# Kernel tuning notes

Hardware: AMD Instinct MI355X
Metric: run time of the kernel (lower is better)

## Reference

```python
import jax, jax.numpy as jnp
import numpy as np

I_FEAT = 4096
O_FEAT = 4096
BATCH = 8192


def setup_inputs() -> dict:
    key = jax.random.key(0)
    k1, k2, k3 = jax.random.split(key, 3)
    x_input = jax.random.normal(k1, (BATCH, I_FEAT), dtype=jnp.float32)
    toeplitz_params = jax.random.normal(k2, (O_FEAT + I_FEAT - 1,), dtype=jnp.float32) * (1.0 / np.sqrt(I_FEAT))
    bias = jax.random.normal(k3, (O_FEAT,), dtype=jnp.float32) * (1.0 / np.sqrt(I_FEAT))
    return {"x_input": x_input, "toeplitz_params": toeplitz_params, "bias": bias}


def _toeplitz(params, out_features, in_features):
    # row i, col j -> params[(out_features - 1 - i) + j]
    i = jnp.arange(out_features)[:, None]
    j = jnp.arange(in_features)[None, :]
    return params[(out_features - 1) - i + j]  # [O, I]


def reference(x_input, toeplitz_params, bias):
    weight = _toeplitz(toeplitz_params, O_FEAT, I_FEAT)  # [O, I]
    # x.mm(weight.t()) + bias
    return jnp.einsum('bi,oi->bo', x_input, weight) + bias[None, :]
```

## Files before the change

### kernel.cpp

```cpp
#include <hip/hip_runtime.h>

typedef __attribute__((ext_vector_type(4))) int i32x4;
typedef __attribute__((ext_vector_type(4))) float f32x4;

#define AS1 __attribute__((address_space(1)))
#define AS3 __attribute__((address_space(3)))

constexpr int MDIM = 8192;
constexpr int NDIM = 4096;
constexpr int KDIM = 4096;

constexpr int BM = 256, BN = 256, BKB = 128;
constexpr int NKT = KDIM / BKB;

__device__ __forceinline__ void gld_lds16(const signed char* g, signed char* l) {
  __builtin_amdgcn_global_load_lds((const AS1 void*)g, (AS3 void*)l, 16, 0, 0);
}

__device__ __forceinline__ int q8(float v, float inv) {
  int q = __float2int_rn(v * inv);
  return q;
}

__global__ void wscale_kernel(const float* __restrict__ params, float* __restrict__ swbuf) {
  int t = (int)threadIdx.x;
  float m = 0.f;
  for (int i = t; i < NDIM + KDIM - 1; i += 256) m = fmaxf(m, fabsf(params[i]));
#pragma unroll
  for (int off = 32; off >= 1; off >>= 1) m = fmaxf(m, __shfl_xor(m, off));
  __shared__ float red[4];
  if ((t & 63) == 0) red[t >> 6] = m;
  __syncthreads();
  if (t == 0) {
    m = fmaxf(fmaxf(red[0], red[1]), fmaxf(red[2], red[3]));
    m = fmaxf(m, 1e-30f);
    swbuf[0] = m * (1.0f / 127.0f);
    swbuf[1] = 127.0f / m;
  }
}

__global__ __launch_bounds__(256) void quant_x_kernel(
    const float* __restrict__ x, signed char* __restrict__ xq, float* __restrict__ sxr) {
  int row = (int)blockIdx.x;
  int t = (int)threadIdx.x;
  const float4* px = (const float4*)(x + (size_t)row * KDIM) + t * 4;
  float4 v[4];
#pragma unroll
  for (int i = 0; i < 4; ++i) v[i] = px[i];
  float m = 0.f;
#pragma unroll
  for (int i = 0; i < 4; ++i)
    m = fmaxf(fmaxf(fmaxf(fabsf(v[i].x), fabsf(v[i].y)), fmaxf(fabsf(v[i].z), fabsf(v[i].w))), m);
#pragma unroll
  for (int off = 32; off >= 1; off >>= 1) m = fmaxf(m, __shfl_xor(m, off));
  __shared__ float red[4];
  if ((t & 63) == 0) red[t >> 6] = m;
  __syncthreads();
  m = fmaxf(fmaxf(red[0], red[1]), fmaxf(red[2], red[3]));
  m = fmaxf(m, 1e-30f);
  float inv = 127.0f / m;
  if (t == 0) sxr[row] = m * (1.0f / 127.0f);
  i32x4 w;
#pragma unroll
  for (int i = 0; i < 4; ++i) {
    int q0 = q8(v[i].x, inv), q1 = q8(v[i].y, inv), q2 = q8(v[i].z, inv), q3 = q8(v[i].w, inv);
    w[i] = (q0 & 0xff) | ((q1 & 0xff) << 8) | ((q2 & 0xff) << 16) | ((q3 & 0xff) << 24);
  }
  *(i32x4*)(xq + (size_t)row * KDIM + t * 16) = w;
}

__global__ __launch_bounds__(256) void build_wq_kernel(
    const float* __restrict__ params, const float* __restrict__ swbuf,
    signed char* __restrict__ wq) {
  float inv = swbuf[1];
  int i = blockIdx.x * 256 + (int)threadIdx.x;
  int o = i >> 8;
  int k0 = (i & 255) << 4;
  const float* p = params + (NDIM - 1 - o + k0);
  i32x4 w;
#pragma unroll
  for (int j = 0; j < 4; ++j) {
    int q0 = q8(p[4 * j + 0], inv), q1 = q8(p[4 * j + 1], inv);
    int q2 = q8(p[4 * j + 2], inv), q3 = q8(p[4 * j + 3], inv);
    w[j] = (q0 & 0xff) | ((q1 & 0xff) << 8) | ((q2 & 0xff) << 16) | ((q3 & 0xff) << 24);
  }
  *(i32x4*)(wq + (size_t)o * KDIM + k0) = w;
}

__global__ __launch_bounds__(512, 2) void toep_gemm_i8(
    const signed char* __restrict__ A,
    const signed char* __restrict__ Bw,
    const float* __restrict__ bias,
    const float* __restrict__ sxr,
    const float* __restrict__ swbuf,
    float* __restrict__ C)
{
  __shared__ signed char sA[2][BM * BKB];
  __shared__ signed char sB[2][BN * BKB];

  constexpr int NBM = MDIM / BM;
  constexpr int NBN = NDIM / BN;
  constexpr int NWG = NBM * NBN;
  int bid = (int)blockIdx.x;
  int swz = (bid & 7) * (NWG >> 3) + (bid >> 3);
  int bm = swz / NBN, bn = swz % NBN;
  int m0 = bm * BM, n0 = bn * BN;

  int t = (int)threadIdx.x;
  int lane = t & 63, wid = t >> 6;
  int wm = wid >> 2, wn = wid & 3;
  int lr = lane & 15, lk = lane >> 4;

  int scol = (((t & 7) ^ ((t >> 3) & 7)) << 4);
  const signed char* gA = A + (size_t)(m0 + (t >> 3)) * KDIM + scol;
  const signed char* gB = Bw + (size_t)(n0 + (t >> 3)) * KDIM + scol;

#define STG_A(c, kt, R0) gld_lds16(gA + (size_t)(R0) * KDIM + (kt) * BKB, &sA[c][(R0) * BKB + t * 16])
#define STG_B(c, kt, R0) gld_lds16(gB + (size_t)(R0) * KDIM + (kt) * BKB, &sB[c][(R0) * BKB + t * 16])

  int aswz = (lr & 7) << 4;
  int c0 = (lk * 16) ^ aswz;
  int c1 = (64 + lk * 16) ^ aswz;

  i32x4 av[4][2], bvA[2][2], bvB[2][2];
  i32x4 acc[8][4];
#pragma unroll
  for (int i = 0; i < 8; ++i)
#pragma unroll
    for (int j = 0; j < 4; ++j) acc[i][j] = (i32x4){0, 0, 0, 0};

#define LDA_SUB(c, msub) do { \
  _Pragma("unroll") \
  for (int mi = 0; mi < 4; ++mi) { \
    const signed char* p_ = &sA[c][(wm * 128 + (msub) * 64 + mi * 16 + lr) * BKB]; \
    av[mi][0] = *(const i32x4*)(p_ + c0); \
    av[mi][1] = *(const i32x4*)(p_ + c1); \
  } } while (0)

#define LDB_GRP(c, nsub, BV) do { \
  _Pragma("unroll") \
  for (int ni = 0; ni < 2; ++ni) { \
    const signed char* p_ = &sB[c][(wn * 64 + (nsub) * 32 + ni * 16 + lr) * BKB]; \
    BV[ni][0] = *(const i32x4*)(p_ + c0); \
    BV[ni][1] = *(const i32x4*)(p_ + c1); \
  } } while (0)

#define MMA_Q(msub, nsub, BV) do { \
  __builtin_amdgcn_s_setprio(1); \
  _Pragma("unroll") \
  for (int mi = 0; mi < 4; ++mi) \
    _Pragma("unroll") \
    for (int ni = 0; ni < 2; ++ni) { \
      acc[(msub) * 4 + mi][(nsub) * 2 + ni] = __builtin_amdgcn_mfma_i32_16x16x64_i8( \
          av[mi][0], BV[ni][0], acc[(msub) * 4 + mi][(nsub) * 2 + ni], 0, 0, 0); \
      acc[(msub) * 4 + mi][(nsub) * 2 + ni] = __builtin_amdgcn_mfma_i32_16x16x64_i8( \
          av[mi][1], BV[ni][1], acc[(msub) * 4 + mi][(nsub) * 2 + ni], 0, 0, 0); \
    } \
  __builtin_amdgcn_s_setprio(0); \
} while (0)

#define SB0() __builtin_amdgcn_sched_barrier(0)
#define BAR() __builtin_amdgcn_s_barrier()

  STG_B(0, 0, 0); STG_B(0, 0, 64); STG_B(0, 0, 128); STG_B(0, 0, 192);
  STG_A(0, 0, 0); STG_A(0, 0, 64); STG_A(0, 0, 128); STG_A(0, 0, 192);
  asm volatile("s_waitcnt vmcnt(0)" ::: "memory");
  BAR();

#define TILE(c, kt) do { \
  const bool st_ = (kt) + 1 < NKT; \
  if (st_) { \
    STG_B((c) ^ 1, (kt) + 1, 0); STG_B((c) ^ 1, (kt) + 1, 64); \
    STG_B((c) ^ 1, (kt) + 1, 128); STG_B((c) ^ 1, (kt) + 1, 192); \
    STG_A((c) ^ 1, (kt) + 1, 0); STG_A((c) ^ 1, (kt) + 1, 64); \
    STG_A((c) ^ 1, (kt) + 1, 128); STG_A((c) ^ 1, (kt) + 1, 192); \
  } \
  LDA_SUB(c, 0); LDB_GRP(c, 0, bvA); SB0(); \
  LDB_GRP(c, 1, bvB); \
  asm volatile("s_waitcnt lgkmcnt(4)" ::: "memory"); SB0(); \
  MMA_Q(0, 0, bvA); \
  asm volatile("s_waitcnt lgkmcnt(0)" ::: "memory"); SB0(); \
  MMA_Q(0, 1, bvB); \
  LDA_SUB(c, 1); \
  asm volatile("s_waitcnt lgkmcnt(0)" ::: "memory"); SB0(); \
  MMA_Q(1, 1, bvB); \
  MMA_Q(1, 0, bvA); \
  asm volatile("s_waitcnt vmcnt(0)" ::: "memory"); \
  BAR(); \
} while (0)

  for (int kt = 0; kt < NKT; kt += 2) {
    TILE(0, kt);
    TILE(1, kt + 1);
  }

  float sw = swbuf[0];
  float bvv[4];
#pragma unroll
  for (int fn = 0; fn < 4; ++fn) bvv[fn] = bias[n0 + wn * 64 + fn * 16 + lr];
#pragma unroll
  for (int fm = 0; fm < 8; ++fm) {
    int row0 = m0 + wm * 128 + fm * 16 + lk * 4;
    float sx_[4];
#pragma unroll
    for (int r = 0; r < 4; ++r) sx_[r] = sxr[row0 + r] * sw;
#pragma unroll
    for (int fn = 0; fn < 4; ++fn) {
      int col = n0 + wn * 64 + fn * 16 + lr;
#pragma unroll
      for (int r = 0; r < 4; ++r)
        C[(size_t)(row0 + r) * NDIM + col] = (float)acc[fm][fn][r] * sx_[r] + bvv[fn];
    }
  }
#undef TILE
#undef MMA_Q
#undef LDB_GRP
#undef LDA_SUB
#undef STG_A
#undef STG_B
#undef SB0
#undef BAR
}

__global__ __launch_bounds__(256) void toep_f32_fallback(
    const float* __restrict__ X, const float* __restrict__ P,
    const float* __restrict__ bias, float* __restrict__ C)
{
  constexpr int TM = 64, TN = 64, TK = 32;
  __shared__ float xs[TM][TK + 1];
  __shared__ float win[TN + TK];
  int bm = blockIdx.x / (NDIM / TN);
  int bn = blockIdx.x % (NDIM / TN);
  int m0 = bm * TM, n0 = bn * TN;
  int t = (int)threadIdx.x;
  int tx = t & 15, ty = t >> 4;
  float acc[4][4] = {};
  for (int k0 = 0; k0 < KDIM; k0 += TK) {
    __syncthreads();
    for (int i = t; i < TM * TK; i += 256) {
      int r = i >> 5, c = i & 31;
      xs[r][c] = X[(size_t)(m0 + r) * KDIM + k0 + c];
    }
    if (t < TN + TK - 1) win[t] = P[(NDIM - 1) - n0 - (TN - 1) + k0 + t];
    __syncthreads();
    for (int kk = 0; kk < TK; ++kk) {
      float xv[4];
#pragma unroll
      for (int i = 0; i < 4; ++i) xv[i] = xs[ty * 4 + i][kk];
#pragma unroll
      for (int j = 0; j < 4; ++j) {
        float wv = win[kk + (TN - 1) - (tx * 4 + j)];
#pragma unroll
        for (int i = 0; i < 4; ++i) acc[i][j] += xv[i] * wv;
      }
    }
  }
#pragma unroll
  for (int i = 0; i < 4; ++i)
#pragma unroll
    for (int j = 0; j < 4; ++j)
      C[(size_t)(m0 + ty * 4 + i) * NDIM + n0 + tx * 4 + j] = acc[i][j] + bias[n0 + tx * 4 + j];
}

extern "C" void kernel_launch(void* const* d_in, const int* in_sizes, int n_in,
                              void* d_out, int out_size, void* d_ws, size_t ws_size,
                              hipStream_t stream) {
  const float* x = (const float*)d_in[0];
  const float* params = (const float*)d_in[1];
  const float* bias = (const float*)d_in[2];
  float* out = (float*)d_out;

  const size_t xq_off = 0;
  const size_t wq_off = (size_t)MDIM * KDIM;
  const size_t sx_off = wq_off + (size_t)NDIM * KDIM;
  const size_t sw_off = sx_off + (size_t)MDIM * 4;
  const size_t need = sw_off + 64;

  if (ws_size >= need) {
    signed char* xq = (signed char*)d_ws + xq_off;
    signed char* wq = (signed char*)d_ws + wq_off;
    float* sxr = (float*)((char*)d_ws + sx_off);
    float* swbuf = (float*)((char*)d_ws + sw_off);
    wscale_kernel<<<1, 256, 0, stream>>>(params, swbuf);
    quant_x_kernel<<<MDIM, 256, 0, stream>>>(x, xq, sxr);
    build_wq_kernel<<<NDIM * KDIM / 16 / 256, 256, 0, stream>>>(params, swbuf, wq);
    toep_gemm_i8<<<(MDIM / BM) * (NDIM / BN), 512, 0, stream>>>(xq, wq, bias, sxr, swbuf, out);
  } else {
    toep_f32_fallback<<<(MDIM / 64) * (NDIM / 64), 256, 0, stream>>>(x, params, bias, out);
  }
}
```

Baseline: 175.9 us.

## Prefetch next tile's LDS fragments across barrier and interleave global staging with MFMA

Adds a second A-fragment register set so the first A/B fragments of the next k-tile are read from LDS right after the barrier, overlapping with the last MFMA quadrant of the current tile. The global-to-LDS staging loads are split into B and A halves placed between MFMA quadrants rather than issued all at once at the start of the tile. The goal is to hide LDS read latency and spread memory issue across compute. In exchange it raises VGPR pressure, which could reduce occupancy or cause spills. The vmcnt waits also become tighter to get right.

Result: no change. 173.6 us (-1.3%).

```diff
diff --git a/kernel.cpp b/kernel.cpp
--- a/kernel.cpp
+++ b/kernel.cpp
@@ -18,8 +18,7 @@
 }
 
 __device__ __forceinline__ int q8(float v, float inv) {
-  int q = __float2int_rn(v * inv);
-  return q;
+  return __float2int_rn(v * inv);
 }
 
 __global__ void wscale_kernel(const float* __restrict__ params, float* __restrict__ swbuf) {
@@ -122,19 +121,20 @@
   int c0 = (lk * 16) ^ aswz;
   int c1 = (64 + lk * 16) ^ aswz;
 
-  i32x4 av[4][2], bvA[2][2], bvB[2][2];
+  i32x4 avA[4][2], avB[4][2];
+  i32x4 bvA[2][2], bvB[2][2];
   i32x4 acc[8][4];
 #pragma unroll
   for (int i = 0; i < 8; ++i)
 #pragma unroll
     for (int j = 0; j < 4; ++j) acc[i][j] = (i32x4){0, 0, 0, 0};
 
-#define LDA_SUB(c, msub) do { \
+#define LDA_GRP(c, msub, AV) do { \
   _Pragma("unroll") \
   for (int mi = 0; mi < 4; ++mi) { \
     const signed char* p_ = &sA[c][(wm * 128 + (msub) * 64 + mi * 16 + lr) * BKB]; \
-    av[mi][0] = *(const i32x4*)(p_ + c0); \
-    av[mi][1] = *(const i32x4*)(p_ + c1); \
+    AV[mi][0] = *(const i32x4*)(p_ + c0); \
+    AV[mi][1] = *(const i32x4*)(p_ + c1); \
   } } while (0)
 
 #define LDB_GRP(c, nsub, BV) do { \
@@ -145,16 +145,16 @@
     BV[ni][1] = *(const i32x4*)(p_ + c1); \
   } } while (0)
 
-#define MMA_Q(msub, nsub, BV) do { \
+#define MMA_Q(msub, nsub, AV, BV) do { \
   __builtin_amdgcn_s_setprio(1); \
   _Pragma("unroll") \
   for (int mi = 0; mi < 4; ++mi) \
     _Pragma("unroll") \
     for (int ni = 0; ni < 2; ++ni) { \
       acc[(msub) * 4 + mi][(nsub) * 2 + ni] = __builtin_amdgcn_mfma_i32_16x16x64_i8( \
-          av[mi][0], BV[ni][0], acc[(msub) * 4 + mi][(nsub) * 2 + ni], 0, 0, 0); \
+          AV[mi][0], BV[ni][0], acc[(msub) * 4 + mi][(nsub) * 2 + ni], 0, 0, 0); \
       acc[(msub) * 4 + mi][(nsub) * 2 + ni] = __builtin_amdgcn_mfma_i32_16x16x64_i8( \
-          av[mi][1], BV[ni][1], acc[(msub) * 4 + mi][(nsub) * 2 + ni], 0, 0, 0); \
+          AV[mi][1], BV[ni][1], acc[(msub) * 4 + mi][(nsub) * 2 + ni], 0, 0, 0); \
     } \
   __builtin_amdgcn_s_setprio(0); \
 } while (0)
@@ -166,27 +166,33 @@
   STG_A(0, 0, 0); STG_A(0, 0, 64); STG_A(0, 0, 128); STG_A(0, 0, 192);
   asm volatile("s_waitcnt vmcnt(0)" ::: "memory");
   BAR();
+  LDA_GRP(0, 0, avA); LDB_GRP(0, 0, bvA);
+  SB0();
 
 #define TILE(c, kt) do { \
   const bool st_ = (kt) + 1 < NKT; \
-  if (st_) { \
-    STG_B((c) ^ 1, (kt) + 1, 0); STG_B((c) ^ 1, (kt) + 1, 64); \
-    STG_B((c) ^ 1, (kt) + 1, 128); STG_B((c) ^ 1, (kt) + 1, 192); \
-    STG_A((c) ^ 1, (kt) + 1, 0); STG_A((c) ^ 1, (kt) + 1, 64); \
-    STG_A((c) ^ 1, (kt) + 1, 128); STG_A((c) ^ 1, (kt) + 1, 192); \
-  } \
-  LDA_SUB(c, 0); LDB_GRP(c, 0, bvA); SB0(); \
+   \
   LDB_GRP(c, 1, bvB); \
+  if (st_) { STG_B((c) ^ 1, (kt) + 1, 0); STG_B((c) ^ 1, (kt) + 1, 64); \
+             STG_B((c) ^ 1, (kt) + 1, 128); STG_B((c) ^ 1, (kt) + 1, 192); } \
+  SB0(); \
   asm volatile("s_waitcnt lgkmcnt(4)" ::: "memory"); SB0(); \
-  MMA_Q(0, 0, bvA); \
+  MMA_Q(0, 0, avA, bvA); \
+   \
+  LDA_GRP(c, 1, avB); \
+  if (st_) { STG_A((c) ^ 1, (kt) + 1, 0); STG_A((c) ^ 1, (kt) + 1, 64); \
+             STG_A((c) ^ 1, (kt) + 1, 128); STG_A((c) ^ 1, (kt) + 1, 192); } \
+  SB0(); \
+  asm volatile("s_waitcnt lgkmcnt(8)" ::: "memory"); SB0(); \
+  MMA_Q(0, 1, avA, bvB); \
+   \
   asm volatile("s_waitcnt lgkmcnt(0)" ::: "memory"); SB0(); \
-  MMA_Q(0, 1, bvB); \
-  LDA_SUB(c, 1); \
-  asm volatile("s_waitcnt lgkmcnt(0)" ::: "memory"); SB0(); \
-  MMA_Q(1, 1, bvB); \
-  MMA_Q(1, 0, bvA); \
-  asm volatile("s_waitcnt vmcnt(0)" ::: "memory"); \
+  MMA_Q(1, 0, avB, bvA); \
+   \
+  if (st_) { asm volatile("s_waitcnt vmcnt(0)" ::: "memory"); } \
   BAR(); \
+  if (st_) { LDA_GRP((c) ^ 1, 0, avA); LDB_GRP((c) ^ 1, 0, bvA); SB0(); } \
+  MMA_Q(1, 1, avB, bvB); \
 } while (0)
 
   for (int kt = 0; kt < NKT; kt += 2) {
@@ -215,7 +221,7 @@
 #undef TILE
 #undef MMA_Q
 #undef LDB_GRP
-#undef LDA_SUB
+#undef LDA_GRP
 #undef STG_A
 #undef STG_B
 #undef SB0
```
